# Performance work log

Hardware: AMD Instinct MI355X
Metric: run time of the kernel (lower is better)

Reference implementation:

```python
import jax, jax.numpy as jnp
import numpy as np

BATCH = 131072
STATE_DIM = 64
CONTROL_DIM = 16
HIDDEN = 256
ALPHA = 0.1
MAX_ITERS = 200
TOL = 0.01
TRACKED_ITERS = 5
U_MIN, U_MAX = -1.0, 1.0


def setup_inputs() -> dict:
    key = jax.random.key(0)
    ks = jax.random.split(key, 8)
    def w(k, shape, fan_in):
        return (jax.random.normal(k, shape, jnp.float32) / np.float32(np.sqrt(fan_in)))
    x = jax.random.normal(ks[0], (BATCH, STATE_DIM), jnp.float32)
    t = jax.random.uniform(ks[1], (1,), jnp.float32)
    W1 = w(ks[2], (STATE_DIM + 1, HIDDEN), STATE_DIM + 1)
    b1 = jnp.zeros((HIDDEN,), jnp.float32)
    W2 = w(ks[3], (HIDDEN, HIDDEN), HIDDEN)
    b2 = jnp.zeros((HIDDEN,), jnp.float32)
    W3 = w(ks[4], (HIDDEN, STATE_DIM), HIDDEN)
    b3 = jnp.zeros((STATE_DIM,), jnp.float32)
    Bmat = w(ks[5], (STATE_DIM, CONTROL_DIM), STATE_DIM)  # oc_problem dynamics matrix
    return {"x": x, "t": t, "W1": W1, "b1": b1, "W2": W2, "b2": b2,
            "W3": W3, "b3": b3, "Bmat": Bmat}


def _p_net(t, x, W1, b1, W2, b2, W3, b3):
    # DefaultPNet: pad x with scalar t, then 3-layer ReLU MLP -> p in [B, state_dim]
    n = x.shape[0]
    tcol = jnp.broadcast_to(t.reshape(1, 1).astype(x.dtype), (n, 1))
    zt = jnp.concatenate([x, tcol], axis=1)
    h = jax.nn.relu(zt @ W1 + b1)
    h = jax.nn.relu(h @ W2 + b2)
    return h @ W3 + b3


def reference(x, t, W1, b1, W2, b2, W3, b3, Bmat):
    # grad_H_u(t,x,u,p) = u + p @ Bmat  (LQ Hamiltonian); p independent of u,
    # so p is computed once (same math as recomputing it every iteration).
    p = _p_net(t, x, W1, b1, W2, b2, W3, b3)          # [B, state_dim]
    pB = p @ Bmat                                      # [B, control_dim]
    clamp = lambda u: jnp.clip(u, U_MIN, U_MAX)
    T = lambda u, pb: u - ALPHA * (u + pb)

    u0 = jnp.zeros((x.shape[0], CONTROL_DIM), x.dtype)
    pB_ng = jax.lax.stop_gradient(pB)

    def cond(st):
        _, i, res = st
        return (res >= TOL) & (i < MAX_ITERS)

    def body(st):
        u, i, _ = st
        u_new = clamp(T(u, pB_ng))
        res = jnp.max(jnp.linalg.norm(u_new - u, axis=1)) / ALPHA
        return (u_new, i + 1, res)

    u_fp, _, _ = jax.lax.while_loop(cond, body, (u0, jnp.int32(0), jnp.float32(jnp.inf)))

    # training path: tracked_iters differentiable refinement steps + final T
    u = jax.lax.stop_gradient(u_fp)
    for _ in range(TRACKED_ITERS + 1):
        u = clamp(T(u, pB))
    return u
```

## Files before the change

kernel.cpp:

```cpp
#include <hip/hip_runtime.h>


typedef __bf16 bf16;
typedef __bf16 bf16x8 __attribute__((ext_vector_type(8)));
typedef __bf16 bf16x4 __attribute__((ext_vector_type(4)));
typedef float  f32x4  __attribute__((ext_vector_type(4)));

#define HID    256
#define SDIM   64
#define CDIM   16
#define BM     128
#define GRID   256
#define ITERS  4

#define OFF_W2P 0
#define OFF_W3P 131072
#define OFF_W1P 139264
#define OFF_B1E 172032
#define OFF_B3B 173056

#define MFMA(a, b, c) __builtin_amdgcn_mfma_f32_16x16x32_bf16(a, b, c, 0, 0, 0)

__device__ __forceinline__ int sh_idx(int row, int h) {
  return (row << 8) + ((((h >> 3) ^ row) & 7) << 3) + (h & 7) + ((h >> 6) << 6);
}

__device__ __forceinline__ int sx_idx(int row, int k) {
  return (row << 6) + ((((k >> 3) ^ row) & 7) << 3) + (k & 7);
}

__global__ __launch_bounds__(512)
void oc_pack(const float* __restrict__ t,  const float* __restrict__ W1,
             const float* __restrict__ b1, const float* __restrict__ W2,
             const float* __restrict__ W3, const float* __restrict__ b3,
             const float* __restrict__ Bmat, char* __restrict__ ws) {
  const int gid = blockIdx.x * 512 + threadIdx.x;
  if (gid < 8192) {
    const int lane = gid & 63, tt = gid >> 6;
    const int nt = tt & 15, kt = tt >> 4;
    const int m = nt * 16 + (lane & 15);
    const int k0 = kt * 32 + ((lane >> 4) << 3);
    bf16x8 v;
#pragma unroll
    for (int j = 0; j < 8; ++j) v[j] = (bf16)W2[(k0 + j) * HID + m];
    *(bf16x8*)((bf16*)(ws + OFF_W2P) + (size_t)gid * 8) = v;
  } else if (gid < 8704) {
    const int e = gid - 8192, kt = e >> 6, fl = e & 63;
    const int r0 = kt * 32 + ((fl >> 4) << 3);
    const int c  = fl & 15;
    float aw[8];
#pragma unroll
    for (int j = 0; j < 8; ++j) aw[j] = 0.f;
    for (int m = 0; m < SDIM; ++m) {
      const float bm = Bmat[m * CDIM + c];
#pragma unroll
      for (int j = 0; j < 8; ++j) aw[j] = fmaf(W3[(r0 + j) * SDIM + m], bm, aw[j]);
    }
    bf16x8 v;
#pragma unroll
    for (int j = 0; j < 8; ++j) v[j] = (bf16)aw[j];
    *(bf16x8*)((bf16*)(ws + OFF_W3P) + (size_t)e * 8) = v;
  } else if (gid < 10752) {
    const int e = gid - 8704;
    const int lane = e & 63, tt = e >> 6;
    const int nt = tt & 15, kt = tt >> 4;
    const int m = nt * 16 + (lane & 15);
    const int k0 = kt * 32 + ((lane >> 4) << 3);
    bf16x8 v;
#pragma unroll
    for (int j = 0; j < 8; ++j) v[j] = (bf16)W1[(k0 + j) * HID + m];
    *(bf16x8*)((bf16*)(ws + OFF_W1P) + (size_t)e * 8) = v;
  } else if (gid < 11008) {
    const int h = gid - 10752;
    ((float*)(ws + OFF_B1E))[h] = b1[h] + t[0] * W1[SDIM * HID + h];
  } else if (gid < 11024) {
    const int c = gid - 11008;
    float s = 0.f;
    for (int m = 0; m < SDIM; ++m) s = fmaf(b3[m], Bmat[m * CDIM + c], s);
    ((float*)(ws + OFF_B3B))[c] = s;
  }
}

__global__ __launch_bounds__(512, 2)
void oc_main(const float* __restrict__ x, const float* __restrict__ b2,
             const char* __restrict__ ws, float* __restrict__ out) {
  __shared__ bf16 sH1[BM * 256];
  __shared__ bf16 sH2[BM * 256];
  __shared__ bf16 sX [BM * 64];
  const int tid  = threadIdx.x;
  const int wave = tid >> 6, lane = tid & 63;
  const int q    = lane >> 4, l = lane & 15;

  const bf16* W2p = (const bf16*)(ws + OFF_W2P);
  const bf16* W3p = (const bf16*)(ws + OFF_W3P);
  const bf16* W1p = (const bf16*)(ws + OFF_W1P);

  {
    const float* xp = x + (size_t)blockIdx.x * BM * SDIM;
#pragma unroll
    for (int i = 0; i < 4; ++i) {
      const int e = i * 512 + tid;
      const int r = e >> 4, k4 = (e & 15) * 4;
      const float4 v = *(const float4*)(xp + r * SDIM + k4);
      bf16x4 w = {(bf16)v.x, (bf16)v.y, (bf16)v.z, (bf16)v.w};
      *(bf16x4*)(&sX[sx_idx(r, k4)]) = w;
    }
  }

  f32x4 b1e[2], b2e[2];
#pragma unroll
  for (int mt = 0; mt < 2; ++mt) {
    const int h0 = 32 * wave + 16 * mt + 4 * q;
    const float4 v1 = *(const float4*)((const float*)(ws + OFF_B1E) + h0);
    const float4 v2 = *(const float4*)(b2 + h0);
    b1e[mt] = (f32x4){v1.x, v1.y, v1.z, v1.w};
    b2e[mt] = (f32x4){v2.x, v2.y, v2.z, v2.w};
  }
  f32x4 b3t;
  {
    const float4 v = *(const float4*)((const float*)(ws + OFF_B3B) + 4 * q);
    b3t = (f32x4){v.x, v.y, v.z, v.w};
  }
  __syncthreads();

  f32x4 acc[2][8];

  for (int it = 0; it < ITERS; ++it) {
    const int tile = blockIdx.x + it * GRID;

#pragma unroll
    for (int mt = 0; mt < 2; ++mt)
#pragma unroll
      for (int nt = 0; nt < 8; ++nt) acc[mt][nt] = b1e[mt];
#pragma unroll
    for (int kt = 0; kt < 2; ++kt) {
      const bf16x8 w1a = *(const bf16x8*)(W1p + ((size_t)(kt * 16 + 2 * wave    ) * 64 + lane) * 8);
      const bf16x8 w1b = *(const bf16x8*)(W1p + ((size_t)(kt * 16 + 2 * wave + 1) * 64 + lane) * 8);
#pragma unroll
      for (int nt = 0; nt < 8; ++nt) {
        const bf16x8 b = *(const bf16x8*)(&sX[sx_idx(16 * nt + l, 32 * kt + 8 * q)]);
        acc[0][nt] = MFMA(w1a, b, acc[0][nt]);
        acc[1][nt] = MFMA(w1b, b, acc[1][nt]);
      }
    }
#pragma unroll
    for (int mt = 0; mt < 2; ++mt) {
      const int h0 = 32 * wave + 16 * mt + 4 * q;
#pragma unroll
      for (int nt = 0; nt < 8; ++nt) {
        bf16x4 v;
#pragma unroll
        for (int r = 0; r < 4; ++r) v[r] = (bf16)fmaxf(acc[mt][nt][r], 0.f);
        *(bf16x4*)(&sH1[sh_idx(16 * nt + l, h0)]) = v;
      }
    }
    __syncthreads();

#pragma unroll
    for (int mt = 0; mt < 2; ++mt)
#pragma unroll
      for (int nt = 0; nt < 8; ++nt) acc[mt][nt] = b2e[mt];
#pragma unroll
    for (int kt = 0; kt < 8; ++kt) {
      const bf16x8 w2a = *(const bf16x8*)(W2p + ((size_t)(kt * 16 + 2 * wave    ) * 64 + lane) * 8);
      const bf16x8 w2b = *(const bf16x8*)(W2p + ((size_t)(kt * 16 + 2 * wave + 1) * 64 + lane) * 8);
#pragma unroll
      for (int nt = 0; nt < 8; ++nt) {
        const bf16x8 b = *(const bf16x8*)(&sH1[sh_idx(16 * nt + l, 32 * kt + 8 * q)]);
        acc[0][nt] = MFMA(w2a, b, acc[0][nt]);
        acc[1][nt] = MFMA(w2b, b, acc[1][nt]);
      }
    }
    __syncthreads();

#pragma unroll
    for (int mt = 0; mt < 2; ++mt) {
      const int h0 = 32 * wave + 16 * mt + 4 * q;
#pragma unroll
      for (int nt = 0; nt < 8; ++nt) {
        bf16x4 hi, lo;
#pragma unroll
        for (int r = 0; r < 4; ++r) {
          const float v = fmaxf(acc[mt][nt][r], 0.f);
          const bf16 h = (bf16)v;
          hi[r] = h;
          lo[r] = (bf16)(v - (float)h);
        }
        const int idx = sh_idx(16 * nt + l, h0);
        *(bf16x4*)(&sH2[idx]) = hi;
        *(bf16x4*)(&sH1[idx]) = lo;
      }
    }
    __syncthreads();

    if (wave < 4) {
#pragma unroll
      for (int g = 0; g < 2; ++g) {
        const int row = 32 * wave + 16 * g + l;
        f32x4 a3 = b3t;
#pragma unroll
        for (int kt = 0; kt < 8; ++kt) {
          const bf16x8 w3 = *(const bf16x8*)(W3p + ((size_t)kt * 64 + lane) * 8);
          const int idx = sh_idx(row, 32 * kt + 8 * q);
          const bf16x8 bh = *(const bf16x8*)(&sH2[idx]);
          const bf16x8 bl = *(const bf16x8*)(&sH1[idx]);
          a3 = MFMA(w3, bh, a3);
          a3 = MFMA(w3, bl, a3);
        }
        f32x4 o;
#pragma unroll
        for (int r = 0; r < 4; ++r)
          o[r] = fminf(fmaxf(-a3[r], -1.f), 1.f);
        *(float4*)(&out[((size_t)tile * BM + row) * CDIM + 4 * q]) = *(float4*)&o;
      }
    } else if (it + 1 < ITERS) {
      const float* xp = x + (size_t)(tile + GRID) * BM * SDIM;
      const int tid2 = tid - 256;
#pragma unroll
      for (int i = 0; i < 8; ++i) {
        const int e = i * 256 + tid2;
        const int r = e >> 4, k4 = (e & 15) * 4;
        const float4 v = *(const float4*)(xp + r * SDIM + k4);
        bf16x4 w = {(bf16)v.x, (bf16)v.y, (bf16)v.z, (bf16)v.w};
        *(bf16x4*)(&sX[sx_idx(r, k4)]) = w;
      }
    }
    __syncthreads();
  }
}

extern "C" void kernel_launch(void* const* d_in, const int* in_sizes, int n_in,
                              void* d_out, int out_size, void* d_ws, size_t ws_size,
                              hipStream_t stream) {
  const float* x    = (const float*)d_in[0];
  const float* t    = (const float*)d_in[1];
  const float* W1   = (const float*)d_in[2];
  const float* b1   = (const float*)d_in[3];
  const float* W2   = (const float*)d_in[4];
  const float* b2   = (const float*)d_in[5];
  const float* W3   = (const float*)d_in[6];
  const float* b3   = (const float*)d_in[7];
  const float* Bmat = (const float*)d_in[8];
  float* out = (float*)d_out;
  char*  ws  = (char*)d_ws;

  hipLaunchKernelGGL(oc_pack, dim3(22), dim3(512), 0, stream,
                     t, W1, b1, W2, W3, b3, Bmat, ws);
  hipLaunchKernelGGL(oc_main, dim3(GRID), dim3(512), 0, stream,
                     x, b2, ws, out);
}
```

Measured before the change: 123.1 us.

## Retile per-wave MFMA work to 64x64 blocks and interleave layer-3 row groups

Each wave now computes a 64-hidden by 64-row tile (4x4 MFMA tiles) instead of 32 hidden by 128 rows. This halves LDS B-fragment reads per MFMA and doubles the register-held weight fragments per k-step. The layer-3 loop is also reordered so one W3 fragment load serves both row groups, giving two independent accumulator chains. Register pressure for weight fragments rises slightly.

```diff
diff --git a/kernel.cpp b/kernel.cpp
--- a/kernel.cpp
+++ b/kernel.cpp
@@ -90,6 +90,8 @@
   const int tid  = threadIdx.x;
   const int wave = tid >> 6, lane = tid & 63;
   const int q    = lane >> 4, l = lane & 15;
+  const int mg   = wave >> 1;
+  const int ng   = wave & 1;
 
   const bf16* W2p = (const bf16*)(ws + OFF_W2P);
   const bf16* W3p = (const bf16*)(ws + OFF_W3P);
@@ -107,10 +109,10 @@
     }
   }
 
-  f32x4 b1e[2], b2e[2];
-#pragma unroll
-  for (int mt = 0; mt < 2; ++mt) {
-    const int h0 = 32 * wave + 16 * mt + 4 * q;
+  f32x4 b1e[4], b2e[4];
+#pragma unroll
+  for (int mt = 0; mt < 4; ++mt) {
+    const int h0 = 64 * mg + 16 * mt + 4 * q;
     const float4 v1 = *(const float4*)((const float*)(ws + OFF_B1E) + h0);
     const float4 v2 = *(const float4*)(b2 + h0);
     b1e[mt] = (f32x4){v1.x, v1.y, v1.z, v1.w};
@@ -123,61 +125,65 @@
   }
   __syncthreads();
 
-  f32x4 acc[2][8];
+  f32x4 acc[4][4];
 
   for (int it = 0; it < ITERS; ++it) {
     const int tile = blockIdx.x + it * GRID;
 
 #pragma unroll
-    for (int mt = 0; mt < 2; ++mt)
-#pragma unroll
-      for (int nt = 0; nt < 8; ++nt) acc[mt][nt] = b1e[mt];
+    for (int mt = 0; mt < 4; ++mt)
+#pragma unroll
+      for (int nt = 0; nt < 4; ++nt) acc[mt][nt] = b1e[mt];
 #pragma unroll
     for (int kt = 0; kt < 2; ++kt) {
-      const bf16x8 w1a = *(const bf16x8*)(W1p + ((size_t)(kt * 16 + 2 * wave    ) * 64 + lane) * 8);
-      const bf16x8 w1b = *(const bf16x8*)(W1p + ((size_t)(kt * 16 + 2 * wave + 1) * 64 + lane) * 8);
-#pragma unroll
-      for (int nt = 0; nt < 8; ++nt) {
-        const bf16x8 b = *(const bf16x8*)(&sX[sx_idx(16 * nt + l, 32 * kt + 8 * q)]);
-        acc[0][nt] = MFMA(w1a, b, acc[0][nt]);
-        acc[1][nt] = MFMA(w1b, b, acc[1][nt]);
-      }
-    }
-#pragma unroll
-    for (int mt = 0; mt < 2; ++mt) {
-      const int h0 = 32 * wave + 16 * mt + 4 * q;
-#pragma unroll
-      for (int nt = 0; nt < 8; ++nt) {
+      bf16x8 w1f[4];
+#pragma unroll
+      for (int mt = 0; mt < 4; ++mt)
+        w1f[mt] = *(const bf16x8*)(W1p + ((size_t)(kt * 16 + 4 * mg + mt) * 64 + lane) * 8);
+#pragma unroll
+      for (int nt = 0; nt < 4; ++nt) {
+        const bf16x8 b = *(const bf16x8*)(&sX[sx_idx(64 * ng + 16 * nt + l, 32 * kt + 8 * q)]);
+#pragma unroll
+        for (int mt = 0; mt < 4; ++mt) acc[mt][nt] = MFMA(w1f[mt], b, acc[mt][nt]);
+      }
+    }
+#pragma unroll
+    for (int mt = 0; mt < 4; ++mt) {
+      const int h0 = 64 * mg + 16 * mt + 4 * q;
+#pragma unroll
+      for (int nt = 0; nt < 4; ++nt) {
         bf16x4 v;
 #pragma unroll
         for (int r = 0; r < 4; ++r) v[r] = (bf16)fmaxf(acc[mt][nt][r], 0.f);
-        *(bf16x4*)(&sH1[sh_idx(16 * nt + l, h0)]) = v;
-      }
-    }
-    __syncthreads();
-
-#pragma unroll
-    for (int mt = 0; mt < 2; ++mt)
-#pragma unroll
-      for (int nt = 0; nt < 8; ++nt) acc[mt][nt] = b2e[mt];
+        *(bf16x4*)(&sH1[sh_idx(64 * ng + 16 * nt + l, h0)]) = v;
+      }
+    }
+    __syncthreads();
+
+#pragma unroll
+    for (int mt = 0; mt < 4; ++mt)
+#pragma unroll
+      for (int nt = 0; nt < 4; ++nt) acc[mt][nt] = b2e[mt];
 #pragma unroll
     for (int kt = 0; kt < 8; ++kt) {
-      const bf16x8 w2a = *(const bf16x8*)(W2p + ((size_t)(kt * 16 + 2 * wave    ) * 64 + lane) * 8);
-      const bf16x8 w2b = *(const bf16x8*)(W2p + ((size_t)(kt * 16 + 2 * wave + 1) * 64 + lane) * 8);
-#pragma unroll
-      for (int nt = 0; nt < 8; ++nt) {
-        const bf16x8 b = *(const bf16x8*)(&sH1[sh_idx(16 * nt + l, 32 * kt + 8 * q)]);
-        acc[0][nt] = MFMA(w2a, b, acc[0][nt]);
-        acc[1][nt] = MFMA(w2b, b, acc[1][nt]);
-      }
-    }
-    __syncthreads();
-
-#pragma unroll
-    for (int mt = 0; mt < 2; ++mt) {
-      const int h0 = 32 * wave + 16 * mt + 4 * q;
-#pragma unroll
-      for (int nt = 0; nt < 8; ++nt) {
+      bf16x8 w2f[4];
+#pragma unroll
+      for (int mt = 0; mt < 4; ++mt)
+        w2f[mt] = *(const bf16x8*)(W2p + ((size_t)(kt * 16 + 4 * mg + mt) * 64 + lane) * 8);
+#pragma unroll
+      for (int nt = 0; nt < 4; ++nt) {
+        const bf16x8 b = *(const bf16x8*)(&sH1[sh_idx(64 * ng + 16 * nt + l, 32 * kt + 8 * q)]);
+#pragma unroll
+        for (int mt = 0; mt < 4; ++mt) acc[mt][nt] = MFMA(w2f[mt], b, acc[mt][nt]);
+      }
+    }
+    __syncthreads();
+
+#pragma unroll
+    for (int mt = 0; mt < 4; ++mt) {
+      const int h0 = 64 * mg + 16 * mt + 4 * q;
+#pragma unroll
+      for (int nt = 0; nt < 4; ++nt) {
         bf16x4 hi, lo;
 #pragma unroll
         for (int r = 0; r < 4; ++r) {
@@ -186,7 +192,7 @@
           hi[r] = h;
           lo[r] = (bf16)(v - (float)h);
         }
-        const int idx = sh_idx(16 * nt + l, h0);
+        const int idx = sh_idx(64 * ng + 16 * nt + l, h0);
         *(bf16x4*)(&sH2[idx]) = hi;
         *(bf16x4*)(&sH1[idx]) = lo;
       }
@@ -194,23 +200,27 @@
     __syncthreads();
 
     if (wave < 4) {
+      f32x4 a3[2];
+      a3[0] = b3t; a3[1] = b3t;
+#pragma unroll
+      for (int kt = 0; kt < 8; ++kt) {
+        const bf16x8 w3 = *(const bf16x8*)(W3p + ((size_t)kt * 64 + lane) * 8);
+#pragma unroll
+        for (int g = 0; g < 2; ++g) {
+          const int idx = sh_idx(32 * wave + 16 * g + l, 32 * kt + 8 * q);
+          const bf16x8 bh = *(const bf16x8*)(&sH2[idx]);
+          const bf16x8 bl = *(const bf16x8*)(&sH1[idx]);
+          a3[g] = MFMA(w3, bh, a3[g]);
+          a3[g] = MFMA(w3, bl, a3[g]);
+        }
+      }
 #pragma unroll
       for (int g = 0; g < 2; ++g) {
         const int row = 32 * wave + 16 * g + l;
-        f32x4 a3 = b3t;
-#pragma unroll
-        for (int kt = 0; kt < 8; ++kt) {
-          const bf16x8 w3 = *(const bf16x8*)(W3p + ((size_t)kt * 64 + lane) * 8);
-          const int idx = sh_idx(row, 32 * kt + 8 * q);
-          const bf16x8 bh = *(const bf16x8*)(&sH2[idx]);
-          const bf16x8 bl = *(const bf16x8*)(&sH1[idx]);
-          a3 = MFMA(w3, bh, a3);
-          a3 = MFMA(w3, bl, a3);
-        }
         f32x4 o;
 #pragma unroll
         for (int r = 0; r < 4; ++r)
-          o[r] = fminf(fmaxf(-a3[r], -1.f), 1.f);
+          o[r] = fminf(fmaxf(-a3[g][r], -1.f), 1.f);
         *(float4*)(&out[((size_t)tile * BM + row) * CDIM + 4 * q]) = *(float4*)&o;
       }
     } else if (it + 1 < ITERS) {
```

Measured after the change: 214.5 us. +74.2%, slower.
